# Optimization experiments

Hardware: AMD Instinct MI355X
Metric: run time of the kernel (lower is better)

Reference implementation:

```python
import jax, jax.numpy as jnp
import numpy as np

SH_C0 = 0.28209479177387814
EPS2D = 0.3      # gsplat low-pass filter added to 2D covariance diagonal
NEAR = 0.01
ALPHA_MIN = 1.0 / 255.0
ALPHA_MAX = 0.999


def setup_inputs() -> dict:
    key = jax.random.key(0)
    ks = jax.random.split(key, 5)
    N = 2048
    means = 0.1 * jax.random.normal(ks[0], (N, 3), jnp.float32)
    quats = jax.random.normal(ks[1], (N, 4), jnp.float32)
    scales = -2.3 + 0.3 * jax.random.normal(ks[2], (N, 3), jnp.float32)
    opacities = -1.0 + 0.5 * jax.random.normal(ks[3], (N,), jnp.float32)
    sh_coeffs = jax.random.normal(ks[4], (N, 1, 3), jnp.float32)
    viewmats = jnp.eye(4, dtype=jnp.float32).at[2, 3].set(2.0)[None]  # [1,4,4] world->cam
    Ks = jnp.array([[[150.0, 0.0, 64.0], [0.0, 150.0, 64.0], [0.0, 0.0, 1.0]]], jnp.float32)
    return dict(means=means, quats=quats, scales=scales, opacities=opacities,
                sh_coeffs=sh_coeffs, viewmats=viewmats, Ks=Ks, width=128, height=128)


def _splat_render(means, quats, scales, opacities, sh_coeffs, viewmats, Ks, width, height):
    # --- parameter activations (GaussianSplat.activated_parameters) ---
    quats = quats / jnp.linalg.norm(quats, axis=-1, keepdims=True)
    scales = jnp.minimum(jnp.exp(scales), 10.0)
    opac = jax.nn.sigmoid(opacities)                                  # [N]
    colors = jnp.maximum(sh_coeffs[:, 0, :] * SH_C0 + 0.5, 0.0)       # [N,3] sh_degree=0

    # --- 3D covariance from quaternion (w,x,y,z) and scale ---
    w, x, y, z = quats[:, 0], quats[:, 1], quats[:, 2], quats[:, 3]
    R = jnp.stack([
        1 - 2 * (y * y + z * z), 2 * (x * y - w * z), 2 * (x * z + w * y),
        2 * (x * y + w * z), 1 - 2 * (x * x + z * z), 2 * (y * z - w * x),
        2 * (x * z - w * y), 2 * (y * z + w * x), 1 - 2 * (x * x + y * y)],
        axis=-1).reshape(-1, 3, 3)                                    # [N,3,3]
    M = R * scales[:, None, :]                                        # R @ diag(s)
    cov3d = jnp.einsum('nij,nkj->nik', M, M)                          # [N,3,3]

    # --- project to camera frame ---
    Rcw = viewmats[:, :3, :3]                                         # [C,3,3]
    tcw = viewmats[:, :3, 3]                                          # [C,3]
    p_cam = jnp.einsum('cij,nj->cni', Rcw, means) + tcw[:, None, :]   # [C,N,3]
    Vc = jnp.einsum('cij,njk,clk->cnil', Rcw, cov3d, Rcw)             # [C,N,3,3]

    xc, yc, zc = p_cam[..., 0], p_cam[..., 1], p_cam[..., 2]
    valid = zc > NEAR
    zs = jnp.where(valid, zc, 1.0)
    rz = 1.0 / zs
    fx = Ks[:, 0, 0][:, None]; fy = Ks[:, 1, 1][:, None]
    cx = Ks[:, 0, 2][:, None]; cy = Ks[:, 1, 2][:, None]
    u = fx * xc * rz + cx                                             # [C,N]
    v = fy * yc * rz + cy

    # --- EWA 2D covariance: J Vc J^T + eps2d*I, J = d(proj)/d(p_cam) ---
    J00 = fx * rz; J02 = -fx * xc * rz * rz
    J11 = fy * rz; J12 = -fy * yc * rz * rz
    V00, V01, V02 = Vc[..., 0, 0], Vc[..., 0, 1], Vc[..., 0, 2]
    V11, V12, V22 = Vc[..., 1, 1], Vc[..., 1, 2], Vc[..., 2, 2]
    a = J00 * J00 * V00 + 2 * J00 * J02 * V02 + J02 * J02 * V22 + EPS2D
    b = J00 * (J11 * V01 + J12 * V02) + J02 * (J11 * V12 + J12 * V22)
    c = J11 * J11 * V11 + 2 * J11 * J12 * V12 + J12 * J12 * V22 + EPS2D
    det = a * c - b * b
    valid = valid & (det > 0)
    det_s = jnp.where(valid, det, 1.0)
    conA = c / det_s; conB = -b / det_s; conC = a / det_s             # conic (inverse cov)

    # --- per-pixel gaussian evaluation (pixel centers at +0.5) ---
    px = jnp.arange(width, dtype=jnp.float32) + 0.5                   # [W]
    py = jnp.arange(height, dtype=jnp.float32) + 0.5                  # [H]
    dx = px[None, None, :] - u[..., None]                             # [C,N,W]
    dy = py[None, None, :] - v[..., None]                             # [C,N,H]
    sigma = (0.5 * (conA[..., None, None] * (dx * dx)[:, :, None, :]
                    + conC[..., None, None] * (dy * dy)[..., None])
             + conB[..., None, None] * dy[..., None] * dx[:, :, None, :])  # [C,N,H,W]
    alpha = opac[None, :, None, None] * jnp.exp(-sigma)
    alpha = jnp.minimum(alpha, ALPHA_MAX)
    alpha = jnp.where(valid[..., None, None] & (alpha >= ALPHA_MIN), alpha, 0.0)

    # --- front-to-back alpha compositing in depth order ---
    order = jnp.argsort(jnp.where(valid, zc, jnp.inf), axis=1)        # [C,N]
    alpha_s = jnp.take_along_axis(alpha, order[:, :, None, None], axis=1)
    colors_s = jnp.take_along_axis(jnp.broadcast_to(colors[None], (alpha.shape[0],) + colors.shape),
                                   order[:, :, None], axis=1)         # [C,N,3]
    logT = jnp.cumsum(jnp.log1p(-alpha_s), axis=1)
    logT_excl = jnp.pad(logT, ((0, 0), (1, 0), (0, 0), (0, 0)))[:, :-1]
    weights = alpha_s * jnp.exp(logT_excl)                            # [C,N,H,W]
    img = jnp.einsum('cnhw,cnk->chwk', weights, colors_s)             # [C,H,W,3]
    return img


def reference(means, quats, scales, opacities, sh_coeffs, viewmats, Ks, width, height):
    return _splat_render(means, quats, scales, opacities, sh_coeffs, viewmats, Ks, width, height)
```

## Files before the change

kernel.cpp:

```cpp
#include <hip/hip_runtime.h>
#include <math.h>

#define SH_C0     0.28209479177387814f
#define EPS2D     0.3f
#define NEARZ     0.01f
#define ALPHA_MIN (1.0f/255.0f)
#define ALPHA_MAX 0.999f
#define LOG2E     1.4426950408889634f

#define SEGS   32
#define LSEG   8
#define NLAYER 4

__global__ __launch_bounds__(256) void prep_rank_kernel(
        const float* __restrict__ means,
        const float* __restrict__ quats,
        const float* __restrict__ scales,
        const float* __restrict__ opacities,
        const float* __restrict__ sh,
        const float* __restrict__ vm,
        const float* __restrict__ K,
        float* __restrict__ sorted,
        int N) {
    int wave = blockIdx.x * 4 + (threadIdx.x >> 6);
    int lane = threadIdx.x & 63;
    if (wave >= N) return;
    int i = wave;

    float r00=vm[0], r01=vm[1], r02=vm[2],  t0=vm[3];
    float r10=vm[4], r11=vm[5], r12=vm[6],  t1=vm[7];
    float r20=vm[8], r21=vm[9], r22=vm[10], t2=vm[11];

    float mx = means[3*i+0], my = means[3*i+1], mz = means[3*i+2];
    float zci = r20*mx + r21*my + r22*mz + t2;
    float keyi = (zci > NEARZ) ? zci : INFINITY;
    int cnt = 0;
    for (int j = lane; j < N; j += 64) {
        float ax = means[3*j+0], ay = means[3*j+1], az = means[3*j+2];
        float zcj = r20*ax + r21*ay + r22*az + t2;
        float keyj = (zcj > NEARZ) ? zcj : INFINITY;
        cnt += (keyj < keyi) || (keyj == keyi && j < i);
    }
    #pragma unroll
    for (int off = 32; off > 0; off >>= 1)
        cnt += __shfl_xor(cnt, off, 64);

    float qw = quats[4*i+0], qx = quats[4*i+1], qy = quats[4*i+2], qz = quats[4*i+3];
    float rqn = rsqrtf(qw*qw + qx*qx + qy*qy + qz*qz);
    qw *= rqn; qx *= rqn; qy *= rqn; qz *= rqn;

    float R00 = 1.f - 2.f*(qy*qy + qz*qz);
    float R01 = 2.f*(qx*qy - qw*qz);
    float R02 = 2.f*(qx*qz + qw*qy);
    float R10 = 2.f*(qx*qy + qw*qz);
    float R11 = 1.f - 2.f*(qx*qx + qz*qz);
    float R12 = 2.f*(qy*qz - qw*qx);
    float R20 = 2.f*(qx*qz - qw*qy);
    float R21 = 2.f*(qy*qz + qw*qx);
    float R22 = 1.f - 2.f*(qx*qx + qy*qy);

    float s0 = fminf(expf(scales[3*i+0]), 10.f);
    float s1 = fminf(expf(scales[3*i+1]), 10.f);
    float s2 = fminf(expf(scales[3*i+2]), 10.f);

    float M00=R00*s0, M01=R01*s1, M02=R02*s2;
    float M10=R10*s0, M11=R11*s1, M12=R12*s2;
    float M20=R20*s0, M21=R21*s1, M22=R22*s2;

    float c00 = M00*M00 + M01*M01 + M02*M02;
    float c01 = M00*M10 + M01*M11 + M02*M12;
    float c02 = M00*M20 + M01*M21 + M02*M22;
    float c11 = M10*M10 + M11*M11 + M12*M12;
    float c12 = M10*M20 + M11*M21 + M12*M22;
    float c22 = M20*M20 + M21*M21 + M22*M22;

    float xc = r00*mx + r01*my + r02*mz + t0;
    float yc = r10*mx + r11*my + r12*mz + t1;
    float zc = zci;

    float T00 = r00*c00 + r01*c01 + r02*c02;
    float T01 = r00*c01 + r01*c11 + r02*c12;
    float T02 = r00*c02 + r01*c12 + r02*c22;
    float T10 = r10*c00 + r11*c01 + r12*c02;
    float T11 = r10*c01 + r11*c11 + r12*c12;
    float T12 = r10*c02 + r11*c12 + r12*c22;
    float T20 = r20*c00 + r21*c01 + r22*c02;
    float T21 = r20*c01 + r21*c11 + r22*c12;
    float T22 = r20*c02 + r21*c12 + r22*c22;
    float V00 = T00*r00 + T01*r01 + T02*r02;
    float V01 = T00*r10 + T01*r11 + T02*r12;
    float V02 = T00*r20 + T01*r21 + T02*r22;
    float V11 = T10*r10 + T11*r11 + T12*r12;
    float V12 = T10*r20 + T11*r21 + T12*r22;
    float V22 = T20*r20 + T21*r21 + T22*r22;

    float fx = K[0], cx = K[2], fy = K[4], cy = K[5];

    bool valid = zc > NEARZ;
    float zs = valid ? zc : 1.0f;
    float rz = 1.0f / zs;
    float u = fx*xc*rz + cx;
    float v = fy*yc*rz + cy;
    float J00 = fx*rz;
    float J02 = -fx*xc*rz*rz;
    float J11 = fy*rz;
    float J12 = -fy*yc*rz*rz;

    float a = J00*J00*V00 + 2.f*J00*J02*V02 + J02*J02*V22 + EPS2D;
    float b = J00*(J11*V01 + J12*V02) + J02*(J11*V12 + J12*V22);
    float c = J11*J11*V11 + 2.f*J11*J12*V12 + J12*J12*V22 + EPS2D;
    float det = a*c - b*b;
    valid = valid && (det > 0.f);
    float det_s = valid ? det : 1.0f;
    float conA =  c / det_s;
    float conB = -b / det_s;
    float conC =  a / det_s;

    float op  = 1.0f / (1.0f + expf(-opacities[i]));
    float cr = fmaxf(sh[3*i+0]*SH_C0 + 0.5f, 0.f);
    float cg = fmaxf(sh[3*i+1]*SH_C0 + 0.5f, 0.f);
    float cb = fmaxf(sh[3*i+2]*SH_C0 + 0.5f, 0.f);

    float e0, e1, e2, e3, e4, e5;
    if (valid) {
        e0 = u; e1 = v;
        e2 = 0.5f*conA*LOG2E; e3 = conB*LOG2E; e4 = 0.5f*conC*LOG2E;
        e5 = op;
    } else {
        e0=0; e1=0; e2=0; e3=0; e4=0; e5=0;
    }

    if (lane < 12) {
        float val;
        switch (lane) {
            case 0:  val = e0; break;
            case 1:  val = e1; break;
            case 2:  val = e2; break;
            case 3:  val = e3; break;
            case 4:  val = e4; break;
            case 5:  val = e5; break;
            case 6:  val = cr; break;
            case 7:  val = cg; break;
            case 8:  val = cb; break;
            default: val = 0.f; break;
        }
        sorted[12*(size_t)cnt + lane] = val;
    }
}

__global__ __launch_bounds__(512, 8) void render_main_kernel(
        const float* __restrict__ sorted,
        float4* __restrict__ parts,
        int N, int P) {
    __shared__ float4 part[LSEG][64];
    int tid  = threadIdx.x;
    int lane = tid & 63;
    int w    = __builtin_amdgcn_readfirstlane(tid >> 6);
    int L    = blockIdx.x & (NLAYER - 1);
    int pg   = blockIdx.x >> 2;
    int p    = pg * 64 + lane;

    float px = (float)(p & 127) + 0.5f;
    float py = (float)(p >> 7) + 0.5f;

    int chunk = (N + SEGS - 1) / SEGS;
    int s  = L * LSEG + w;
    int g0 = s * chunk;
    int g1 = min(g0 + chunk, N);

    const float4* rec = (const float4*)sorted + 3*(size_t)g0;

    float accr = 0.f, accg = 0.f, accb = 0.f, T = 1.f;
    #pragma unroll 2
    for (int g = g0; g < g1; ++g) {
        float4 r0 = rec[0];
        float4 r1 = rec[1];
        float  cb = rec[2].x;
        rec += 3;
        float dx = px - r0.x, dy = py - r0.y;
        float t2 = fmaf(r0.z, dx, r0.w * dy);
        float m  = dx * t2;
        float arg = fmaf(-r1.x, dy*dy, -m);
        float al = r1.y * __builtin_amdgcn_exp2f(arg);
        al = fminf(al, ALPHA_MAX);
        al = (al >= ALPHA_MIN) ? al : 0.f;
        float wgt = T * al;
        accr = fmaf(wgt, r1.z, accr);
        accg = fmaf(wgt, r1.w, accg);
        accb = fmaf(wgt, cb,  accb);
        T = fmaf(-al, T, T);
    }
    part[w][lane] = make_float4(accr, accg, accb, T);
    __syncthreads();

    if (tid < 64) {
        float R = 0.f, G = 0.f, Bc = 0.f, Tr = 1.f;
        #pragma unroll
        for (int ss = 0; ss < LSEG; ++ss) {
            float4 q = part[ss][tid];
            R  = fmaf(Tr, q.x, R);
            G  = fmaf(Tr, q.y, G);
            Bc = fmaf(Tr, q.z, Bc);
            Tr *= q.w;
        }
        parts[(size_t)L * P + p] = make_float4(R, G, Bc, Tr);
    }
}

__global__ __launch_bounds__(256) void combine_kernel(
        const float4* __restrict__ parts,
        float* __restrict__ out, int P) {
    int p = blockIdx.x * 256 + threadIdx.x;
    if (p >= P) return;
    float R = 0.f, G = 0.f, B = 0.f, Tr = 1.f;
    #pragma unroll
    for (int l = 0; l < NLAYER; ++l) {
        float4 q = parts[(size_t)l * P + p];
        R  = fmaf(Tr, q.x, R);
        G  = fmaf(Tr, q.y, G);
        B  = fmaf(Tr, q.z, B);
        Tr *= q.w;
    }
    out[3*(size_t)p+0] = R;
    out[3*(size_t)p+1] = G;
    out[3*(size_t)p+2] = B;
}

extern "C" void kernel_launch(void* const* d_in, const int* in_sizes, int n_in,
                              void* d_out, int out_size, void* d_ws, size_t ws_size,
                              hipStream_t stream) {
    const float* means     = (const float*)d_in[0];
    const float* quats     = (const float*)d_in[1];
    const float* scales    = (const float*)d_in[2];
    const float* opacities = (const float*)d_in[3];
    const float* sh        = (const float*)d_in[4];
    const float* vm        = (const float*)d_in[5];
    const float* K         = (const float*)d_in[6];

    int N = in_sizes[0] / 3;
    int P = out_size / 3;

    float*  sorted = (float*)d_ws;
    float4* parts  = (float4*)((float*)d_ws + (size_t)N * 12);

    prep_rank_kernel<<<(N + 3) / 4, 256, 0, stream>>>(
        means, quats, scales, opacities, sh, vm, K, sorted, N);
    render_main_kernel<<<((P + 63) / 64) * NLAYER, 512, 0, stream>>>(
        sorted, parts, N, P);
    combine_kernel<<<(P + 255) / 256, 256, 0, stream>>>(
        parts, (float*)d_out, P);
}
```

Baseline: 95.46 us.

## Render by 8x8 tiles with per-Gaussian bounding-box culling via ballot

The prep kernel now computes a screen-space extent for each Gaussian from its opacity-dependent cutoff radius and marks invisible ones with far-off centres. The renderer switches to one block per 8x8 pixel tile. Each wave tests a slice of sorted Gaussians against the tile bounds, ballots the hits, and evaluates only those, then composes the per-wave partials in shared memory and writes the output directly. This removes the layered partial buffer and the separate combine kernel. The exchange is serialized ballot loops with scalar-indexed loads and a fixed 16x16 tile grid hardcoded for a 128x128 image.

```diff
diff --git a/kernel.cpp b/kernel.cpp
--- a/kernel.cpp
+++ b/kernel.cpp
@@ -7,10 +7,6 @@
 #define ALPHA_MIN (1.0f/255.0f)
 #define ALPHA_MAX 0.999f
 #define LOG2E     1.4426950408889634f
-
-#define SEGS   32
-#define LSEG   8
-#define NLAYER 4
 
 __global__ __launch_bounds__(256) void prep_rank_kernel(
         const float* __restrict__ means,
@@ -121,109 +117,118 @@
     float cg = fmaxf(sh[3*i+1]*SH_C0 + 0.5f, 0.f);
     float cb = fmaxf(sh[3*i+2]*SH_C0 + 0.5f, 0.f);
 
+    float smax = logf(op * 255.0f);
+    bool vis = valid && (smax > 0.f);
+    float denom = conA*conC - conB*conB;
+    float rxe = 0.f, rye = 0.f;
+    if (vis) {
+        float inv = 2.f * smax / denom;
+        rxe = sqrtf(fmaxf(inv * conC, 0.f)) + 0.5f;
+        rye = sqrtf(fmaxf(inv * conA, 0.f)) + 0.5f;
+    }
+
     float e0, e1, e2, e3, e4, e5;
-    if (valid) {
+    if (vis) {
         e0 = u; e1 = v;
         e2 = 0.5f*conA*LOG2E; e3 = conB*LOG2E; e4 = 0.5f*conC*LOG2E;
         e5 = op;
     } else {
-        e0=0; e1=0; e2=0; e3=0; e4=0; e5=0;
+        e0 = -1.0e9f; e1 = -1.0e9f; e2=0; e3=0; e4=0; e5=0;
     }
 
     if (lane < 12) {
         float val;
         switch (lane) {
-            case 0:  val = e0; break;
-            case 1:  val = e1; break;
-            case 2:  val = e2; break;
-            case 3:  val = e3; break;
-            case 4:  val = e4; break;
-            case 5:  val = e5; break;
-            case 6:  val = cr; break;
-            case 7:  val = cg; break;
-            case 8:  val = cb; break;
+            case 0:  val = e0;  break;
+            case 1:  val = e1;  break;
+            case 2:  val = e2;  break;
+            case 3:  val = e3;  break;
+            case 4:  val = e4;  break;
+            case 5:  val = e5;  break;
+            case 6:  val = cr;  break;
+            case 7:  val = cg;  break;
+            case 8:  val = cb;  break;
+            case 9:  val = rxe; break;
+            case 10: val = rye; break;
             default: val = 0.f; break;
         }
         sorted[12*(size_t)cnt + lane] = val;
     }
 }
 
-__global__ __launch_bounds__(512, 8) void render_main_kernel(
-        const float* __restrict__ sorted,
-        float4* __restrict__ parts,
-        int N, int P) {
-    __shared__ float4 part[LSEG][64];
+__global__ __launch_bounds__(512, 2) void render_tile_kernel(
+        const float4* __restrict__ rec,
+        float* __restrict__ out,
+        int N) {
+    __shared__ float4 part[8][64];
     int tid  = threadIdx.x;
     int lane = tid & 63;
-    int w    = __builtin_amdgcn_readfirstlane(tid >> 6);
-    int L    = blockIdx.x & (NLAYER - 1);
-    int pg   = blockIdx.x >> 2;
-    int p    = pg * 64 + lane;
-
-    float px = (float)(p & 127) + 0.5f;
-    float py = (float)(p >> 7) + 0.5f;
-
-    int chunk = (N + SEGS - 1) / SEGS;
-    int s  = L * LSEG + w;
-    int g0 = s * chunk;
-    int g1 = min(g0 + chunk, N);
-
-    const float4* rec = (const float4*)sorted + 3*(size_t)g0;
+    int w    = tid >> 6;
+    int t    = blockIdx.x;
+    int tx   = (t & 15) << 3;
+    int ty   = (t >> 4) << 3;
+
+    float px = (float)(tx + (lane & 7)) + 0.5f;
+    float py = (float)(ty + (lane >> 3)) + 0.5f;
+    float x0 = (float)tx + 0.5f, x1 = (float)tx + 7.5f;
+    float y0 = (float)ty + 0.5f, y1 = (float)ty + 7.5f;
+
+    int nwords = (N + 63) >> 6;
+    int wpw    = (nwords + 7) >> 3;
 
     float accr = 0.f, accg = 0.f, accb = 0.f, T = 1.f;
-    #pragma unroll 2
-    for (int g = g0; g < g1; ++g) {
-        float4 r0 = rec[0];
-        float4 r1 = rec[1];
-        float  cb = rec[2].x;
-        rec += 3;
-        float dx = px - r0.x, dy = py - r0.y;
-        float t2 = fmaf(r0.z, dx, r0.w * dy);
-        float m  = dx * t2;
-        float arg = fmaf(-r1.x, dy*dy, -m);
-        float al = r1.y * __builtin_amdgcn_exp2f(arg);
-        al = fminf(al, ALPHA_MAX);
-        al = (al >= ALPHA_MIN) ? al : 0.f;
-        float wgt = T * al;
-        accr = fmaf(wgt, r1.z, accr);
-        accg = fmaf(wgt, r1.w, accg);
-        accb = fmaf(wgt, cb,  accb);
-        T = fmaf(-al, T, T);
+    for (int k = 0; k < wpw; ++k) {
+        int word = w * wpw + k;
+        int base = word << 6;
+        int g = base + lane;
+        bool pred = false;
+        if (g < N) {
+            float4 a0 = rec[3*(size_t)g];
+            float4 a2 = rec[3*(size_t)g + 2];
+            pred = (a0.x + a2.y >= x0) && (a0.x - a2.y <= x1) &&
+                   (a0.y + a2.z >= y0) && (a0.y - a2.z <= y1);
+        }
+        unsigned long long m = __ballot(pred);
+        while (m) {
+            int b = (int)__builtin_ctzll(m);
+            m &= (m - 1);
+            const float4* r = rec + 3*(size_t)(base + b);
+            float4 r0 = r[0];
+            float4 r1 = r[1];
+            float  cb = r[2].x;
+            float dx = px - r0.x, dy = py - r0.y;
+            float t2  = fmaf(r0.z, dx, r0.w * dy);
+            float arg = fmaf(-r1.x, dy*dy, -dx*t2);
+            float al  = r1.y * __builtin_amdgcn_exp2f(arg);
+            al = fminf(al, ALPHA_MAX);
+            al = (al >= ALPHA_MIN) ? al : 0.f;
+            float wg = T * al;
+            accr = fmaf(wg, r1.z, accr);
+            accg = fmaf(wg, r1.w, accg);
+            accb = fmaf(wg, cb,  accb);
+            T = fmaf(-al, T, T);
+        }
     }
     part[w][lane] = make_float4(accr, accg, accb, T);
     __syncthreads();
 
     if (tid < 64) {
-        float R = 0.f, G = 0.f, Bc = 0.f, Tr = 1.f;
+        float R = 0.f, G = 0.f, B = 0.f, Tr = 1.f;
         #pragma unroll
-        for (int ss = 0; ss < LSEG; ++ss) {
-            float4 q = part[ss][tid];
+        for (int s = 0; s < 8; ++s) {
+            float4 q = part[s][tid];
             R  = fmaf(Tr, q.x, R);
             G  = fmaf(Tr, q.y, G);
-            Bc = fmaf(Tr, q.z, Bc);
+            B  = fmaf(Tr, q.z, B);
             Tr *= q.w;
         }
-        parts[(size_t)L * P + p] = make_float4(R, G, Bc, Tr);
-    }
-}
-
-__global__ __launch_bounds__(256) void combine_kernel(
-        const float4* __restrict__ parts,
-        float* __restrict__ out, int P) {
-    int p = blockIdx.x * 256 + threadIdx.x;
-    if (p >= P) return;
-    float R = 0.f, G = 0.f, B = 0.f, Tr = 1.f;
-    #pragma unroll
-    for (int l = 0; l < NLAYER; ++l) {
-        float4 q = parts[(size_t)l * P + p];
-        R  = fmaf(Tr, q.x, R);
-        G  = fmaf(Tr, q.y, G);
-        B  = fmaf(Tr, q.z, B);
-        Tr *= q.w;
-    }
-    out[3*(size_t)p+0] = R;
-    out[3*(size_t)p+1] = G;
-    out[3*(size_t)p+2] = B;
+        int x = tx + (tid & 7);
+        int y = ty + (tid >> 3);
+        int p = y * 128 + x;
+        out[3*(size_t)p+0] = R;
+        out[3*(size_t)p+1] = G;
+        out[3*(size_t)p+2] = B;
+    }
 }
 
 extern "C" void kernel_launch(void* const* d_in, const int* in_sizes, int n_in,
@@ -238,15 +243,11 @@
     const float* K         = (const float*)d_in[6];
 
     int N = in_sizes[0] / 3;
-    int P = out_size / 3;
-
-    float*  sorted = (float*)d_ws;
-    float4* parts  = (float4*)((float*)d_ws + (size_t)N * 12);
+
+    float* sorted = (float*)d_ws;
 
     prep_rank_kernel<<<(N + 3) / 4, 256, 0, stream>>>(
         means, quats, scales, opacities, sh, vm, K, sorted, N);
-    render_main_kernel<<<((P + 63) / 64) * NLAYER, 512, 0, stream>>>(
-        sorted, parts, N, P);
-    combine_kernel<<<(P + 255) / 256, 256, 0, stream>>>(
-        parts, (float*)d_out, P);
+    render_tile_kernel<<<256, 512, 0, stream>>>(
+        (const float4*)sorted, (float*)d_out, N);
 }
```

Result: slower. 109.6 us (+14.8%).
